# Kernel optimization log

Measured on AMD Instinct MI355X. Metric: run time of the kernel, lower is better.

## Reference

```python
import jax, jax.numpy as jnp
import numpy as np

DIL = (1, 2, 4)      # dilation_rates
SEG = (512, 512, 512)  # segment_sizes
H = 16               # num_heads
D = 1024             # d_model
B, L = 2, 8192


def _mha(x, Wqkv, bqkv, Wo, bo):
    # x: [..., S, D]; standard self-attention (FlashMHA math)
    lead = x.shape[:-2]
    S = x.shape[-2]
    hd = D // H
    qkv = x @ Wqkv.T + bqkv                      # [..., S, 3D]
    q, k, v = jnp.split(qkv, 3, axis=-1)
    q = q.reshape(*lead, S, H, hd)
    k = k.reshape(*lead, S, H, hd)
    v = v.reshape(*lead, S, H, hd)
    scale = 1.0 / np.float32(np.sqrt(hd))
    scores = jnp.einsum('...qhd,...khd->...hqk', q, k) * scale
    a = jax.nn.softmax(scores, axis=-1)
    o = jnp.einsum('...hqk,...khd->...qhd', a, v).reshape(*lead, S, D)
    return o @ Wo.T + bo


def setup_inputs() -> dict:
    key = jax.random.key(0)
    ks = jax.random.split(key, 5)
    n = len(DIL)
    x = jax.random.normal(ks[0], (B, L, D), dtype=jnp.float32)
    Wqkv = 0.02 * jax.random.normal(ks[1], (n, 3 * D, D), dtype=jnp.float32)
    bqkv = jnp.zeros((n, 3 * D), dtype=jnp.float32)
    Wout = 0.02 * jax.random.normal(ks[2], (n, D, D), dtype=jnp.float32)
    bout = jnp.zeros((n, D), dtype=jnp.float32)
    return {"x": x, "Wqkv": Wqkv, "bqkv": bqkv, "Wout": Wout, "bout": bout}


def reference(x, Wqkv, bqkv, Wout, bout):
    b_, L_, D_ = x.shape
    n = len(DIL)
    # Faithful to the original: zip(weights, all_head_outputs) truncates to the
    # first n = len(dilation_rates) of the (branch, offset) outputs.
    pairs = [(br, off) for br in range(n) for off in range(DIL[br])][:n]
    outs = []
    for br, off in pairs:
        r, S = DIL[br], SEG[br]
        xs = x[:, off::r, :].reshape(b_, -1, S, D_)   # [B, n_seg, S, D]
        att = _mha(xs, Wqkv[br], bqkv[br], Wout[br], bout[br])
        full = jnp.zeros_like(x).at[:, off::r, :].set(att.reshape(b_, -1, D_))
        outs.append(full)
    w = jax.nn.softmax(jnp.full((n,), 1.0 / n, dtype=x.dtype))  # uniform -> 1/n each
    res = outs[0] * w[0]
    for i in range(1, n):
        res = res + w[i] * outs[i]
    return res
```

## Files before the change

### kernel.cpp

```cpp
#include <hip/hip_runtime.h>
#include <math.h>

#define TOK    16384
#define DMODEL 1024
#define H3     3072
#define QKD    2048
#define LSEQ   8192
#define CHUNK  8192

typedef unsigned short ushort_t;
using bf16x8 = __attribute__((ext_vector_type(8))) __bf16;
using us8    = __attribute__((ext_vector_type(8))) unsigned short;
using f32x4  = __attribute__((ext_vector_type(4))) float;

__device__ __forceinline__ unsigned short f2bf(float f) {
    unsigned int u = __float_as_uint(f);
    u += 0x7FFF + ((u >> 16) & 1);
    return (unsigned short)(u >> 16);
}
__device__ __forceinline__ float bf2f(unsigned short b) {
    return __uint_as_float(((unsigned int)b) << 16);
}
__device__ __forceinline__ bf16x8 us8_to_bf(us8 u) {
    union { us8 u; bf16x8 b; } t; t.u = u; return t.b;
}

__device__ __forceinline__ void gld16(const void* g, void* l) {
    __builtin_amdgcn_global_load_lds(
        (const __attribute__((address_space(1))) unsigned int*)g,
        (__attribute__((address_space(3))) unsigned int*)l, 16, 0, 0);
}

__global__ __launch_bounds__(256) void split_f32(
    const float* __restrict__ s, ushort_t* __restrict__ h,
    ushort_t* __restrict__ l, int n4, int perm)
{
    int i = blockIdx.x * 256 + threadIdx.x;
    if (i >= n4) return;
    int src = i;
    if (perm) {
        int row = i >> 8, col = i & 255;
        int chunk = row >> 13, p = row & 8191;
        int orow = (chunk << 13) + ((p & 4095) * 2 + (p >> 12));
        src = orow * 256 + col;
    }
    float4 v = ((const float4*)s)[src];
    ushort4 hp, lp;
    hp.x = f2bf(v.x); lp.x = f2bf(v.x - bf2f(hp.x));
    hp.y = f2bf(v.y); lp.y = f2bf(v.y - bf2f(hp.y));
    hp.z = f2bf(v.z); lp.z = f2bf(v.z - bf2f(hp.z));
    hp.w = f2bf(v.w); lp.w = f2bf(v.w - bf2f(hp.w));
    ((ushort4*)h)[i] = hp;
    ((ushort4*)l)[i] = lp;
}

__global__ __launch_bounds__(256, 2) void gemm_split_nt(
    const ushort_t* __restrict__ Ah, const ushort_t* __restrict__ Al,
    const ushort_t* __restrict__ Wh, const ushort_t* __restrict__ Wl,
    const float* __restrict__ bias, float* __restrict__ C,
    ushort_t* __restrict__ Ch, ushort_t* __restrict__ Cl,
    ushort_t* __restrict__ Vth, ushort_t* __restrict__ Vtl,
    int M, int N, int K, float scale, int beta, int qkv_mode)
{
    __shared__ __align__(16) ushort_t As[2][16 * 512];
    __shared__ __align__(16) ushort_t Bs[2][8 * 512];

    const int tid  = threadIdx.x;
    const int lane = tid & 63;
    const int w    = tid >> 6;
    const int m0 = blockIdx.y * 256;
    const int n0 = blockIdx.x * 128;

    long soA[4], soB[2];
#pragma unroll
    for (int i = 0; i < 4; ++i) {
        int row = m0 + (w * 4 + i) * 16 + (lane & 15);
        soA[i] = (long)row * K + (lane >> 4) * 8;
    }
#pragma unroll
    for (int i = 0; i < 2; ++i) {
        int row = n0 + (w * 2 + i) * 16 + (lane & 15);
        soB[i] = (long)row * K + (lane >> 4) * 8;
    }
    ushort_t* dAh = As[0] + (w * 4) * 512;
    ushort_t* dAl = As[1] + (w * 4) * 512;
    ushort_t* dBh = Bs[0] + (w * 2) * 512;
    ushort_t* dBl = Bs[1] + (w * 2) * 512;

    const int am0 = (w >> 1) * 8;
    const int bn0 = (w & 1) * 4;

    f32x4 acc[8][4];
#pragma unroll
    for (int i = 0; i < 8; ++i)
#pragma unroll
        for (int j = 0; j < 4; ++j) acc[i][j] = (f32x4){0.f, 0.f, 0.f, 0.f};

    for (int k0 = 0; k0 < K; k0 += 32) {
#pragma unroll
        for (int i = 0; i < 4; ++i) {
            gld16(Ah + soA[i] + k0, dAh + i * 512);
            gld16(Al + soA[i] + k0, dAl + i * 512);
        }
#pragma unroll
        for (int i = 0; i < 2; ++i) {
            gld16(Wh + soB[i] + k0, dBh + i * 512);
            gld16(Wl + soB[i] + k0, dBl + i * 512);
        }
        __syncthreads();

        bf16x8 bh[4], bl[4];
#pragma unroll
        for (int j = 0; j < 4; ++j) {
            bh[j] = *(const bf16x8*)(Bs[0] + (bn0 + j) * 512 + lane * 8);
            bl[j] = *(const bf16x8*)(Bs[1] + (bn0 + j) * 512 + lane * 8);
        }
#pragma unroll
        for (int i = 0; i < 8; ++i) {
            const bf16x8 ah = *(const bf16x8*)(As[0] + (am0 + i) * 512 + lane * 8);
            const bf16x8 al = *(const bf16x8*)(As[1] + (am0 + i) * 512 + lane * 8);
#pragma unroll
            for (int j = 0; j < 4; ++j)
                acc[i][j] = __builtin_amdgcn_mfma_f32_16x16x32_bf16(
                    ah, bh[j], acc[i][j], 0, 0, 0);
#pragma unroll
            for (int j = 0; j < 4; ++j)
                acc[i][j] = __builtin_amdgcn_mfma_f32_16x16x32_bf16(
                    al, bh[j], acc[i][j], 0, 0, 0);
#pragma unroll
            for (int j = 0; j < 4; ++j)
                acc[i][j] = __builtin_amdgcn_mfma_f32_16x16x32_bf16(
                    ah, bl[j], acc[i][j], 0, 0, 0);
        }
        __syncthreads();
    }

    const int wm = (w >> 1) * 128, wn = (w & 1) * 64;
    const int r0 = (lane >> 4) * 4;
    const int cn = lane & 15;

    if (qkv_mode) {
        const bool isV = (n0 >= 1024 * 2);
#pragma unroll
        for (int j = 0; j < 4; ++j) {
            int col = n0 + wn + j * 16 + cn;
            float bv = bias[col];
#pragma unroll
            for (int i = 0; i < 8; ++i) {
                int rowb = m0 + wm + i * 16 + r0;
                if (isV) {
                    unsigned short ha[4], la[4];
#pragma unroll
                    for (int r = 0; r < 4; ++r) {
                        float v = acc[i][j][r] + bv;
                        ha[r] = f2bf(v);
                        la[r] = f2bf(v - bf2f(ha[r]));
                    }
                    size_t vidx = (size_t)(col - 2048) * M + rowb;
                    *(ushort4*)(Vth + vidx) = make_ushort4(ha[0], ha[1], ha[2], ha[3]);
                    *(ushort4*)(Vtl + vidx) = make_ushort4(la[0], la[1], la[2], la[3]);
                } else {
#pragma unroll
                    for (int r = 0; r < 4; ++r) {
                        float v = acc[i][j][r] + bv;
                        unsigned short hb = f2bf(v);
                        size_t idx = (size_t)(rowb + r) * QKD + col;
                        Ch[idx] = hb;
                        Cl[idx] = f2bf(v - bf2f(hb));
                    }
                }
            }
        }
    } else {
#pragma unroll
        for (int j = 0; j < 4; ++j) {
            int col = n0 + wn + j * 16 + cn;
            float bv = bias[col];
#pragma unroll
            for (int i = 0; i < 8; ++i) {
                int rowb = m0 + wm + i * 16 + r0;
#pragma unroll
                for (int r = 0; r < 4; ++r) {
                    size_t idx = (size_t)(rowb + r) * N + col;
                    float v = scale * (acc[i][j][r] + bv);
                    C[idx] = beta ? (C[idx] + v) : v;
                }
            }
        }
    }
}

__global__ __launch_bounds__(256) void attn_mfma(
    const ushort_t* __restrict__ qkh, const ushort_t* __restrict__ qkl,
    const ushort_t* __restrict__ vth, const ushort_t* __restrict__ vtl,
    ushort_t* __restrict__ aoh, ushort_t* __restrict__ aol,
    int perm, long tok0)
{
    __shared__ __align__(16) ushort_t Kls[2][4096];
    __shared__ __align__(16) ushort_t Vls[2][4096];
    __shared__ __align__(16) float    Ps[4][16 * 68];

    const int tid  = threadIdx.x;
    const int lane = tid & 63;
    const int w    = tid >> 6;
    const int l15  = lane & 15;
    const int lg   = lane >> 4;
    const int qt = blockIdx.x, h = blockIdx.y, z = blockIdx.z;
    const int base = z * 512;

    bf16x8 qh[2], ql[2];
    {
        const int qrow = base + qt * 64 + w * 16 + l15;
        const size_t rb = (size_t)qrow * QKD + h * 64 + lg * 8;
        qh[0] = *(const bf16x8*)(qkh + rb);
        ql[0] = *(const bf16x8*)(qkl + rb);
        qh[1] = *(const bf16x8*)(qkh + rb + 32);
        ql[1] = *(const bf16x8*)(qkl + rb + 32);
    }

    const bool isV = (w >> 1) != 0;
    const int  jm  = (w & 1) * 2;
    const ushort_t* srcH = isV ? vth : qkh;
    const ushort_t* srcL = isV ? vtl : qkl;
    size_t so[4];
    ushort_t *dH[4], *dL[4];
#pragma unroll
    for (int dj = 0; dj < 2; ++dj)
#pragma unroll
        for (int ks = 0; ks < 2; ++ks) {
            const int j = jm + dj, idx = dj * 2 + ks;
            if (!isV)
                so[idx] = (size_t)(base + 16 * j + l15) * QKD + 1024 + h * 64 + 32 * ks + lg * 8;
            else
                so[idx] = (size_t)(h * 64 + 16 * j + l15) * CHUNK + base + 32 * ks + lg * 8;
            dH[idx] = (isV ? Vls[0] : Kls[0]) + (j * 2 + ks) * 512;
            dL[idx] = (isV ? Vls[1] : Kls[1]) + (j * 2 + ks) * 512;
        }
    const size_t kstep = isV ? 64 : (size_t)64 * QKD;

    f32x4 oacc[4];
#pragma unroll
    for (int j = 0; j < 4; ++j) oacc[j] = (f32x4){0.f, 0.f, 0.f, 0.f};
    float m_r[4] = {-INFINITY, -INFINITY, -INFINITY, -INFINITY};
    float l_r[4] = {0.f, 0.f, 0.f, 0.f};
    float* const pw = Ps[w];

    for (int kt = 0; kt < 8; ++kt) {
#pragma unroll
        for (int i = 0; i < 4; ++i) {
            gld16(srcH + so[i], dH[i]);
            gld16(srcL + so[i], dL[i]);
            so[i] += kstep;
        }
        __syncthreads();

        f32x4 s[4];
#pragma unroll
        for (int j = 0; j < 4; ++j) s[j] = (f32x4){0.f, 0.f, 0.f, 0.f};
#pragma unroll
        for (int j = 0; j < 4; ++j)
#pragma unroll
            for (int ks = 0; ks < 2; ++ks) {
                const bf16x8 kh = *(const bf16x8*)(&Kls[0][(j * 2 + ks) * 512 + lane * 8]);
                const bf16x8 kl = *(const bf16x8*)(&Kls[1][(j * 2 + ks) * 512 + lane * 8]);
                s[j] = __builtin_amdgcn_mfma_f32_16x16x32_bf16(qh[ks], kh, s[j], 0, 0, 0);
                s[j] = __builtin_amdgcn_mfma_f32_16x16x32_bf16(ql[ks], kh, s[j], 0, 0, 0);
                s[j] = __builtin_amdgcn_mfma_f32_16x16x32_bf16(qh[ks], kl, s[j], 0, 0, 0);
            }

        float alpha[4];
#pragma unroll
        for (int r = 0; r < 4; ++r) {
            float v = fmaxf(fmaxf(s[0][r], s[1][r]), fmaxf(s[2][r], s[3][r]));
            v = fmaxf(v, __shfl_xor(v, 1));
            v = fmaxf(v, __shfl_xor(v, 2));
            v = fmaxf(v, __shfl_xor(v, 4));
            v = fmaxf(v, __shfl_xor(v, 8));
            const float mn = fmaxf(m_r[r], 0.125f * v);
            alpha[r] = __expf(m_r[r] - mn);
            m_r[r] = mn;
            float sum = 0.f;
#pragma unroll
            for (int j = 0; j < 4; ++j) {
                const float p = __expf(fmaf(0.125f, s[j][r], -mn));
                s[j][r] = p;
                sum += p;
            }
            sum += __shfl_xor(sum, 1);
            sum += __shfl_xor(sum, 2);
            sum += __shfl_xor(sum, 4);
            sum += __shfl_xor(sum, 8);
            l_r[r] = l_r[r] * alpha[r] + sum;
        }

#pragma unroll
        for (int r = 0; r < 4; ++r)
#pragma unroll
            for (int j = 0; j < 4; ++j)
                pw[(lg * 4 + r) * 68 + 16 * j + l15] = s[j][r];
        asm volatile("s_waitcnt lgkmcnt(0)" ::: "memory");
        __builtin_amdgcn_sched_barrier(0);

#pragma unroll
        for (int j = 0; j < 4; ++j)
#pragma unroll
            for (int r = 0; r < 4; ++r) oacc[j][r] *= alpha[r];

#pragma unroll
        for (int ks = 0; ks < 2; ++ks) {
            const float* pp = pw + l15 * 68 + ks * 32 + lg * 8;
            const float4 pa = *(const float4*)pp;
            const float4 pb = *(const float4*)(pp + 4);
            const float pf[8] = {pa.x, pa.y, pa.z, pa.w, pb.x, pb.y, pb.z, pb.w};
            us8 hu, lu;
#pragma unroll
            for (int e = 0; e < 8; ++e) {
                const unsigned short hb = f2bf(pf[e]);
                hu[e] = hb;
                lu[e] = f2bf(pf[e] - bf2f(hb));
            }
            const bf16x8 ph = us8_to_bf(hu);
            const bf16x8 pl = us8_to_bf(lu);
#pragma unroll
            for (int j = 0; j < 4; ++j) {
                const bf16x8 vh = *(const bf16x8*)(&Vls[0][(j * 2 + ks) * 512 + lane * 8]);
                const bf16x8 vl = *(const bf16x8*)(&Vls[1][(j * 2 + ks) * 512 + lane * 8]);
                oacc[j] = __builtin_amdgcn_mfma_f32_16x16x32_bf16(ph, vh, oacc[j], 0, 0, 0);
                oacc[j] = __builtin_amdgcn_mfma_f32_16x16x32_bf16(pl, vh, oacc[j], 0, 0, 0);
                oacc[j] = __builtin_amdgcn_mfma_f32_16x16x32_bf16(ph, vl, oacc[j], 0, 0, 0);
            }
        }
        __syncthreads();
    }

    float linv[4];
#pragma unroll
    for (int r = 0; r < 4; ++r) linv[r] = 1.f / l_r[r];
#pragma unroll
    for (int j = 0; j < 4; ++j)
#pragma unroll
        for (int r = 0; r < 4; ++r)
            pw[(lg * 4 + r) * 68 + 16 * j + l15] = oacc[j][r] * linv[r];
    asm volatile("s_waitcnt lgkmcnt(0)" ::: "memory");
    __builtin_amdgcn_sched_barrier(0);

    {
        const int rr = lane >> 2, c0 = (lane & 3) * 16;
        const float* rp = pw + rr * 68 + c0;
        const int p_local = base + qt * 64 + w * 16 + rr;
        const long tok = tok0 + (perm ? (long)((p_local & 4095) * 2 + (p_local >> 12))
                                      : (long)p_local);
        const size_t off = (size_t)tok * DMODEL + h * 64 + c0;
        const float4 f0 = *(const float4*)rp;
        const float4 f1 = *(const float4*)(rp + 4);
        const float4 f2 = *(const float4*)(rp + 8);
        const float4 f3 = *(const float4*)(rp + 12);
        const float ff[16] = {f0.x, f0.y, f0.z, f0.w, f1.x, f1.y, f1.z, f1.w,
                              f2.x, f2.y, f2.z, f2.w, f3.x, f3.y, f3.z, f3.w};
        us8 h0, h1, l0, l1;
#pragma unroll
        for (int e = 0; e < 8; ++e) {
            unsigned short hb = f2bf(ff[e]);
            h0[e] = hb; l0[e] = f2bf(ff[e] - bf2f(hb));
            hb = f2bf(ff[e + 8]);
            h1[e] = hb; l1[e] = f2bf(ff[e + 8] - bf2f(hb));
        }
        *(us8*)(aoh + off)     = h0;
        *(us8*)(aoh + off + 8) = h1;
        *(us8*)(aol + off)     = l0;
        *(us8*)(aol + off + 8) = l1;
    }
}

extern "C" void kernel_launch(void* const* d_in, const int* in_sizes, int n_in,
                              void* d_out, int out_size, void* d_ws, size_t ws_size,
                              hipStream_t stream) {
    const float* x    = (const float*)d_in[0];
    const float* Wqkv = (const float*)d_in[1];
    const float* bqkv = (const float*)d_in[2];
    const float* Wout = (const float*)d_in[3];
    const float* bout = (const float*)d_in[4];
    float* out = (float*)d_out;

    char* wp = (char*)d_ws;
    ushort_t* xh  = (ushort_t*)wp; wp += (size_t)TOK * DMODEL * 2;
    ushort_t* xl  = (ushort_t*)wp; wp += (size_t)TOK * DMODEL * 2;
    ushort_t* wqh = (ushort_t*)wp; wp += (size_t)H3 * DMODEL * 2;
    ushort_t* wql = (ushort_t*)wp; wp += (size_t)H3 * DMODEL * 2;
    ushort_t* woh = (ushort_t*)wp; wp += (size_t)DMODEL * DMODEL * 2;
    ushort_t* wol = (ushort_t*)wp; wp += (size_t)DMODEL * DMODEL * 2;
    ushort_t* qkh = (ushort_t*)wp; wp += (size_t)CHUNK * QKD * 2;
    ushort_t* qkl = (ushort_t*)wp; wp += (size_t)CHUNK * QKD * 2;
    ushort_t* vth = (ushort_t*)wp; wp += (size_t)DMODEL * CHUNK * 2;
    ushort_t* vtl = (ushort_t*)wp; wp += (size_t)DMODEL * CHUNK * 2;
    ushort_t* aoh = (ushort_t*)wp; wp += (size_t)TOK * DMODEL * 2;
    ushort_t* aol = (ushort_t*)wp;

    dim3 blk(256);
    const float third = 1.0f / 3.0f;

    for (int br = 0; br < 2; ++br) {
        {
            int n4x = TOK * DMODEL / 4;
            split_f32<<<(n4x + 255) / 256, blk, 0, stream>>>(x, xh, xl, n4x, br);
            int n4q = H3 * DMODEL / 4;
            split_f32<<<(n4q + 255) / 256, blk, 0, stream>>>(
                Wqkv + (size_t)br * H3 * DMODEL, wqh, wql, n4q, 0);
            int n4o = DMODEL * DMODEL / 4;
            split_f32<<<(n4o + 255) / 256, blk, 0, stream>>>(
                Wout + (size_t)br * DMODEL * DMODEL, woh, wol, n4o, 0);
        }
        for (int c = 0; c < TOK / CHUNK; ++c) {
            gemm_split_nt<<<dim3(H3 / 128, CHUNK / 256), blk, 0, stream>>>(
                xh + (size_t)c * CHUNK * DMODEL, xl + (size_t)c * CHUNK * DMODEL,
                wqh, wql, bqkv + (size_t)br * H3, nullptr,
                qkh, qkl, vth, vtl,
                CHUNK, H3, DMODEL, 1.0f, 0, 1);
            attn_mfma<<<dim3(8, 16, 16), blk, 0, stream>>>(
                qkh, qkl, vth, vtl, aoh, aol, br, (long)c * CHUNK);
        }
        gemm_split_nt<<<dim3(DMODEL / 128, TOK / 256), blk, 0, stream>>>(
            aoh, aol, woh, wol, bout + (size_t)br * DMODEL, out,
            nullptr, nullptr, nullptr, nullptr,
            TOK, DMODEL, DMODEL, third, br, 0);
    }
}
```

Baseline: 1.728 ms.

## Double-buffer LDS in split-bf16 GEMM and swizzle workgroup order

Adds a second LDS buffer so global-to-LDS loads for the next K-slice are issued while MFMAs run on the current one, replacing two barriers per iteration with one waitcnt-plus-barrier. The block index is remapped with a stride-8 swizzle to change which tiles run concurrently, aiming at better L2 reuse. LDS doubles, so launch bounds drop to one block per CU, trading occupancy for overlap within the block. The loop assumes K is a multiple of 32, and the swizzle assumes the grid size is divisible by 8.

Result: slower. 2.068 ms (+19.6%).

```diff
diff --git a/kernel.cpp b/kernel.cpp
--- a/kernel.cpp
+++ b/kernel.cpp
@@ -54,7 +54,7 @@
     ((ushort4*)l)[i] = lp;
 }
 
-__global__ __launch_bounds__(256, 2) void gemm_split_nt(
+__global__ __launch_bounds__(256, 1) void gemm_split_nt(
     const ushort_t* __restrict__ Ah, const ushort_t* __restrict__ Al,
     const ushort_t* __restrict__ Wh, const ushort_t* __restrict__ Wl,
     const float* __restrict__ bias, float* __restrict__ C,
@@ -62,14 +62,20 @@
     ushort_t* __restrict__ Vth, ushort_t* __restrict__ Vtl,
     int M, int N, int K, float scale, int beta, int qkv_mode)
 {
-    __shared__ __align__(16) ushort_t As[2][16 * 512];
-    __shared__ __align__(16) ushort_t Bs[2][8 * 512];
+    __shared__ __align__(16) ushort_t As[2][2][16 * 512];
+    __shared__ __align__(16) ushort_t Bs[2][2][8 * 512];
 
     const int tid  = threadIdx.x;
     const int lane = tid & 63;
     const int w    = tid >> 6;
-    const int m0 = blockIdx.y * 256;
-    const int n0 = blockIdx.x * 128;
+
+    const int nwg = gridDim.x * gridDim.y;
+    const int id  = blockIdx.y * gridDim.x + blockIdx.x;
+    const int swz = (id & 7) * (nwg >> 3) + (id >> 3);
+    const int bx  = swz % gridDim.x;
+    const int by  = swz / gridDim.x;
+    const int m0 = by * 256;
+    const int n0 = bx * 128;
 
     long soA[4], soB[2];
 #pragma unroll
@@ -82,10 +88,6 @@
         int row = n0 + (w * 2 + i) * 16 + (lane & 15);
         soB[i] = (long)row * K + (lane >> 4) * 8;
     }
-    ushort_t* dAh = As[0] + (w * 4) * 512;
-    ushort_t* dAl = As[1] + (w * 4) * 512;
-    ushort_t* dBh = Bs[0] + (w * 2) * 512;
-    ushort_t* dBl = Bs[1] + (w * 2) * 512;
 
     const int am0 = (w >> 1) * 8;
     const int bn0 = (w & 1) * 4;
@@ -96,44 +98,68 @@
 #pragma unroll
         for (int j = 0; j < 4; ++j) acc[i][j] = (f32x4){0.f, 0.f, 0.f, 0.f};
 
-    for (int k0 = 0; k0 < K; k0 += 32) {
-#pragma unroll
-        for (int i = 0; i < 4; ++i) {
-            gld16(Ah + soA[i] + k0, dAh + i * 512);
-            gld16(Al + soA[i] + k0, dAl + i * 512);
-        }
-#pragma unroll
-        for (int i = 0; i < 2; ++i) {
-            gld16(Wh + soB[i] + k0, dBh + i * 512);
-            gld16(Wl + soB[i] + k0, dBl + i * 512);
-        }
-        __syncthreads();
-
-        bf16x8 bh[4], bl[4];
-#pragma unroll
-        for (int j = 0; j < 4; ++j) {
-            bh[j] = *(const bf16x8*)(Bs[0] + (bn0 + j) * 512 + lane * 8);
-            bl[j] = *(const bf16x8*)(Bs[1] + (bn0 + j) * 512 + lane * 8);
-        }
-#pragma unroll
-        for (int i = 0; i < 8; ++i) {
-            const bf16x8 ah = *(const bf16x8*)(As[0] + (am0 + i) * 512 + lane * 8);
-            const bf16x8 al = *(const bf16x8*)(As[1] + (am0 + i) * 512 + lane * 8);
-#pragma unroll
-            for (int j = 0; j < 4; ++j)
-                acc[i][j] = __builtin_amdgcn_mfma_f32_16x16x32_bf16(
-                    ah, bh[j], acc[i][j], 0, 0, 0);
-#pragma unroll
-            for (int j = 0; j < 4; ++j)
-                acc[i][j] = __builtin_amdgcn_mfma_f32_16x16x32_bf16(
-                    al, bh[j], acc[i][j], 0, 0, 0);
-#pragma unroll
-            for (int j = 0; j < 4; ++j)
-                acc[i][j] = __builtin_amdgcn_mfma_f32_16x16x32_bf16(
-                    ah, bl[j], acc[i][j], 0, 0, 0);
-        }
-        __syncthreads();
-    }
+#define STAGE(b, k0)                                                     \
+    {                                                                    \
+        ushort_t* dAh_ = As[b][0] + (w * 4) * 512;                       \
+        ushort_t* dAl_ = As[b][1] + (w * 4) * 512;                       \
+        ushort_t* dBh_ = Bs[b][0] + (w * 2) * 512;                       \
+        ushort_t* dBl_ = Bs[b][1] + (w * 2) * 512;                       \
+        _Pragma("unroll")                                                \
+        for (int i = 0; i < 4; ++i) {                                    \
+            gld16(Ah + soA[i] + (k0), dAh_ + i * 512);                   \
+            gld16(Al + soA[i] + (k0), dAl_ + i * 512);                   \
+        }                                                                \
+        _Pragma("unroll")                                                \
+        for (int i = 0; i < 2; ++i) {                                    \
+            gld16(Wh + soB[i] + (k0), dBh_ + i * 512);                   \
+            gld16(Wl + soB[i] + (k0), dBl_ + i * 512);                   \
+        }                                                                \
+    }
+
+#define COMPUTE(b)                                                       \
+    {                                                                    \
+        bf16x8 bh[4], bl[4];                                             \
+        _Pragma("unroll")                                                \
+        for (int j = 0; j < 4; ++j) {                                    \
+            bh[j] = *(const bf16x8*)(Bs[b][0] + (bn0 + j) * 512 + lane * 8); \
+            bl[j] = *(const bf16x8*)(Bs[b][1] + (bn0 + j) * 512 + lane * 8); \
+        }                                                                \
+        _Pragma("unroll")                                                \
+        for (int i = 0; i < 8; ++i) {                                    \
+            const bf16x8 ah = *(const bf16x8*)(As[b][0] + (am0 + i) * 512 + lane * 8); \
+            const bf16x8 al = *(const bf16x8*)(As[b][1] + (am0 + i) * 512 + lane * 8); \
+            _Pragma("unroll")                                            \
+            for (int j = 0; j < 4; ++j)                                  \
+                acc[i][j] = __builtin_amdgcn_mfma_f32_16x16x32_bf16(     \
+                    ah, bh[j], acc[i][j], 0, 0, 0);                      \
+            _Pragma("unroll")                                            \
+            for (int j = 0; j < 4; ++j)                                  \
+                acc[i][j] = __builtin_amdgcn_mfma_f32_16x16x32_bf16(     \
+                    al, bh[j], acc[i][j], 0, 0, 0);                      \
+            _Pragma("unroll")                                            \
+            for (int j = 0; j < 4; ++j)                                  \
+                acc[i][j] = __builtin_amdgcn_mfma_f32_16x16x32_bf16(     \
+                    ah, bl[j], acc[i][j], 0, 0, 0);                      \
+        }                                                                \
+    }
+
+#define WB()                                                             \
+    asm volatile("s_waitcnt vmcnt(0)" ::: "memory");                     \
+    __builtin_amdgcn_s_barrier();
+
+    STAGE(0, 0);
+    WB();
+    for (int k0 = 32; k0 < K; k0 += 64) {
+        STAGE(1, k0);
+        COMPUTE(0);
+        WB();
+        if (k0 + 32 < K) { STAGE(0, k0 + 32); }
+        COMPUTE(1);
+        if (k0 + 32 < K) { WB(); }
+    }
+#undef STAGE
+#undef COMPUTE
+#undef WB
 
     const int wm = (w >> 1) * 128, wn = (w & 1) * 64;
     const int r0 = (lane >> 4) * 4;
```
